# Optimization experiments

Hardware: AMD Instinct MI355X
Metric: run time of the kernel (lower is better)

The kernel has to match this reference:

```python
import jax, jax.numpy as jnp
import numpy as np

N_HEADS = 16
N_KV_HEADS = 4
HEAD_DIM = 128


def apply_rotary_emb(x, cos, sin):
    # x: [B, S, H, D]; cos/sin: [S, D//2]
    xr = x[..., 0::2]
    xi = x[..., 1::2]
    c = cos[None, :, None, :]
    s = sin[None, :, None, :]
    out_r = xr * c - xi * s
    out_i = xr * s + xi * c
    # interleave back: [..., D//2, 2] -> [..., D]
    return jnp.stack([out_r, out_i], axis=-1).reshape(x.shape)


def setup_inputs() -> dict:
    key = jax.random.key(0)
    ks = jax.random.split(key, 7)
    B, S, D = 4, 2048, 2048
    x = jax.random.normal(ks[0], (B, S, D), dtype=jnp.float32)
    # realistic rotary tables
    inv_freq = 1.0 / (10000.0 ** (jnp.arange(0, HEAD_DIM, 2, dtype=jnp.float32) / HEAD_DIM))
    t = jnp.arange(S, dtype=jnp.float32)
    freqs = jnp.outer(t, inv_freq)  # [S, D/2]
    freqs_cos = jnp.cos(freqs)
    freqs_sin = jnp.sin(freqs)
    sc = 0.02
    wq = jax.random.normal(ks[1], (D, N_HEADS * HEAD_DIM), dtype=jnp.float32) * sc
    wk = jax.random.normal(ks[2], (D, N_KV_HEADS * HEAD_DIM), dtype=jnp.float32) * sc
    wv = jax.random.normal(ks[3], (D, N_KV_HEADS * HEAD_DIM), dtype=jnp.float32) * sc
    wo = jax.random.normal(ks[4], (N_HEADS * HEAD_DIM, D), dtype=jnp.float32) * sc
    return {"x": x, "freqs_cos": freqs_cos, "freqs_sin": freqs_sin,
            "wq": wq, "wk": wk, "wv": wv, "wo": wo}


def reference(x, freqs_cos, freqs_sin, wq, wk, wv, wo):
    B, S, D = x.shape
    n_rep = N_HEADS // N_KV_HEADS
    xq = (x @ wq).reshape(B, S, N_HEADS, HEAD_DIM)
    xk = (x @ wk).reshape(B, S, N_KV_HEADS, HEAD_DIM)
    xv = (x @ wv).reshape(B, S, N_KV_HEADS, HEAD_DIM)
    xq = apply_rotary_emb(xq, freqs_cos, freqs_sin)
    xk = apply_rotary_emb(xk, freqs_cos, freqs_sin)
    # repeat_kv (GQA): [B,S,Hkv,D] -> [B,S,Hkv*n_rep,D]
    xk = jnp.repeat(xk, n_rep, axis=2)
    xv = jnp.repeat(xv, n_rep, axis=2)
    # [B,H,S,D]
    q = xq.transpose(0, 2, 1, 3)
    k = xk.transpose(0, 2, 1, 3)
    v = xv.transpose(0, 2, 1, 3)
    scores = jnp.einsum('bhqd,bhkd->bhqk', q, k) / jnp.sqrt(jnp.float32(HEAD_DIM))
    causal = jnp.triu(jnp.ones((S, S), dtype=bool), k=1)
    scores = jnp.where(causal[None, None], -jnp.inf, scores)
    probs = jax.nn.softmax(scores, axis=-1)
    out = jnp.einsum('bhqk,bhkd->bhqd', probs, v)
    out = out.transpose(0, 2, 1, 3).reshape(B, S, N_HEADS * HEAD_DIM)
    return out @ wo
```

## Files before the change

kernel.cpp:

```cpp
#include <hip/hip_runtime.h>
#include <stdint.h>
#include <stddef.h>

#define B_ 4
#define S_ 2048
#define D_ 2048
#define NH 16
#define NKV 4
#define HD 128
#define QKV_N 3072
#define ROWS (B_*S_)

typedef unsigned short u16;
typedef __attribute__((ext_vector_type(8))) unsigned short u16x8;
typedef __attribute__((ext_vector_type(8))) __bf16 bf16x8;
typedef __attribute__((ext_vector_type(4))) float f32x4;

__device__ __forceinline__ u16 f2bf(float f) {
  unsigned u = __builtin_bit_cast(unsigned, f);
  return (u16)((u + 0x7fffu + ((u >> 16) & 1u)) >> 16);
}
__device__ __forceinline__ float bf2f(u16 h) {
  return __builtin_bit_cast(float, (unsigned)h << 16);
}
__device__ __forceinline__ f32x4 mfma16(u16x8 a, u16x8 b, f32x4 c) {
  return __builtin_amdgcn_mfma_f32_16x16x32_bf16(
      __builtin_bit_cast(bf16x8, a), __builtin_bit_cast(bf16x8, b), c, 0, 0, 0);
}
__device__ __forceinline__ void gld16(const void* g, void* l) {
  __builtin_amdgcn_global_load_lds(
      (const __attribute__((address_space(1))) void*)g,
      (__attribute__((address_space(3))) void*)l, 16, 0, 0);
}

__global__ __launch_bounds__(256) void k_cast_x(const float* __restrict__ x, u16* __restrict__ xb) {
  int i = blockIdx.x * 256 + threadIdx.x;
  float4 v = ((const float4*)x)[i];
  union { u16 u[4]; uint2 p; } o;
  o.u[0] = f2bf(v.x); o.u[1] = f2bf(v.y); o.u[2] = f2bf(v.z); o.u[3] = f2bf(v.w);
  ((uint2*)xb)[i] = o.p;
}

__global__ __launch_bounds__(256) void k_wt(const float* __restrict__ w, u16* __restrict__ wt, int K, int N) {
  __shared__ float tile[32][33];
  int kb = blockIdx.y * 32, nb = blockIdx.x * 32;
  int tx = threadIdx.x, ty = threadIdx.y;
#pragma unroll
  for (int j = 0; j < 32; j += 8)
    tile[ty + j][tx] = w[(size_t)(kb + ty + j) * N + nb + tx];
  __syncthreads();
#pragma unroll
  for (int j = 0; j < 32; j += 8)
    wt[(size_t)(nb + ty + j) * K + kb + tx] = f2bf(tile[tx][ty + j]);
}

template<int NT, bool F32OUT>
__global__ __launch_bounds__(256) void k_gemm(const u16* __restrict__ A, const u16* __restrict__ Bt,
                                              void* __restrict__ C) {
  const int K = 2048;
  __shared__ u16 As[128 * 32];
  __shared__ u16 Bs[128 * 32];
  int mb = blockIdx.y * 128, nb = blockIdx.x * 128;
  int t = threadIdx.x;
  int l = t & 63, lane16 = l & 15, quad = l >> 4;
  int w = t >> 6;
  int wm = (w >> 1) * 64, wn = (w & 1) * 64;
  f32x4 acc[4][4] = {};
  for (int k0 = 0; k0 < K; k0 += 32) {
#pragma unroll
    for (int p = 0; p < 2; ++p) {
      int lin = p * 256 + t;
      int row = lin >> 2, ch = lin & 3;
      gld16(A  + (size_t)(mb + row) * K + k0 + ch * 8, As + (p * 256 + (t & 192)) * 8);
      gld16(Bt + (size_t)(nb + row) * K + k0 + ch * 8, Bs + (p * 256 + (t & 192)) * 8);
    }
    __syncthreads();
    u16x8 af[4], bf[4];
#pragma unroll
    for (int mt = 0; mt < 4; ++mt)
      af[mt] = *(const u16x8*)(As + (wm + mt * 16 + lane16) * 32 + quad * 8);
#pragma unroll
    for (int nt = 0; nt < 4; ++nt)
      bf[nt] = *(const u16x8*)(Bs + (wn + nt * 16 + lane16) * 32 + quad * 8);
#pragma unroll
    for (int mt = 0; mt < 4; ++mt)
#pragma unroll
      for (int nt = 0; nt < 4; ++nt)
        acc[mt][nt] = mfma16(af[mt], bf[nt], acc[mt][nt]);
    __syncthreads();
  }
#pragma unroll
  for (int mt = 0; mt < 4; ++mt)
#pragma unroll
    for (int nt = 0; nt < 4; ++nt)
#pragma unroll
      for (int r = 0; r < 4; ++r) {
        int row = mb + wm + mt * 16 + quad * 4 + r;
        int col = nb + wn + nt * 16 + lane16;
        if constexpr (F32OUT)
          ((float*)C)[(size_t)row * NT + col] = acc[mt][nt][r];
        else
          ((u16*)C)[(size_t)row * NT + col] = f2bf(acc[mt][nt][r]);
      }
}

__global__ __launch_bounds__(256) void k_rope(const u16* __restrict__ qkv, const float* __restrict__ fc,
                                              const float* __restrict__ fs, u16* __restrict__ Q,
                                              u16* __restrict__ Kk) {
  const float SC = 0.1275174214f;
  int row = blockIdx.x;
  int b = row >> 11, s = row & 2047;
  int t = threadIdx.x;
#pragma unroll
  for (int j = 0; j < 5; ++j) {
    int p = t + j * 256;
    int i = p & 63;
    float c = fc[s * 64 + i], sn = fs[s * 64 + i];
    if (p < 1024) {
      int h = p >> 6;
      unsigned pr = *(const unsigned*)(qkv + (size_t)row * QKV_N + h * 128 + 2 * i);
      float xr = bf2f((u16)(pr & 0xffff)), xi = bf2f((u16)(pr >> 16));
      size_t o = (((size_t)(b * NH + h) * S_) + s) * HD + 2 * i;
      unsigned out = (unsigned)f2bf((xr * c - xi * sn) * SC) |
                     ((unsigned)f2bf((xr * sn + xi * c) * SC) << 16);
      *(unsigned*)(Q + o) = out;
    } else {
      int kh = (p - 1024) >> 6;
      unsigned pr = *(const unsigned*)(qkv + (size_t)row * QKV_N + 2048 + kh * 128 + 2 * i);
      float xr = bf2f((u16)(pr & 0xffff)), xi = bf2f((u16)(pr >> 16));
      size_t o = (((size_t)(b * NKV + kh) * S_) + s) * HD + 2 * i;
      unsigned out = (unsigned)f2bf(xr * c - xi * sn) | ((unsigned)f2bf(xr * sn + xi * c) << 16);
      *(unsigned*)(Kk + o) = out;
    }
  }
}

__global__ __launch_bounds__(256) void k_vt(const u16* __restrict__ qkv, u16* __restrict__ Vt) {
  __shared__ u16 tile[64 * 128];
  int blk = blockIdx.x;
  int sb = blk & 31, kh = (blk >> 5) & 3, b = blk >> 7;
  int t = threadIdx.x;
  int s0 = sb * 64;
#pragma unroll
  for (int i = 0; i < 4; ++i) {
    int lin = i * 256 + t;
    int row = lin >> 4, c = lin & 15;
    u16x8 v = *(const u16x8*)(qkv + (size_t)(b * S_ + s0 + row) * QKV_N + 2560 + kh * HD + c * 8);
    *(u16x8*)(tile + row * 128 + ((c ^ (row & 15)) * 8)) = v;
  }
  __syncthreads();
#pragma unroll
  for (int i = 0; i < 2; ++i) {
    int u = i * 256 + t;
    int p = u >> 3, o = u & 7;
    u16 lo[8], hi[8];
#pragma unroll
    for (int j = 0; j < 8; ++j) {
      int s = o * 8 + j;
      int cs = (p >> 2) ^ (s & 15);
      unsigned v = *(const unsigned*)(tile + s * 128 + cs * 8 + (p & 3) * 2);
      lo[j] = (u16)(v & 0xffff); hi[j] = (u16)(v >> 16);
    }
    size_t ob = ((size_t)(b * NKV + kh) * HD + 2 * p) * S_ + s0 + o * 8;
    *(u16x8*)(Vt + ob)      = *(u16x8*)lo;
    *(u16x8*)(Vt + ob + S_) = *(u16x8*)hi;
  }
}

__global__ __launch_bounds__(256) void k_attn(const u16* __restrict__ Q, const u16* __restrict__ Kg,
                                              const u16* __restrict__ Vt, u16* __restrict__ O) {
  int bx = blockIdx.x;
  int bh = bx >> 3, pr = bx & 7;
  int b = bh >> 4, h = bh & 15, kh = h >> 2;
  int t = threadIdx.x;
  int w = t >> 6, l = t & 63, L = l & 15, quad = l >> 4;

  __shared__ u16 Ks[64 * 128];
  __shared__ u16 Vs[128 * 64];
  __shared__ u16 Ps[4][32 * 72];
  u16* Pw = &Ps[w][0];

  const u16* Qh = Q  + ((size_t)(b * NH  + h ) * S_) * HD;
  const u16* Kh = Kg + ((size_t)(b * NKV + kh) * S_) * HD;
  const u16* Vh = Vt + ((size_t)(b * NKV + kh) * HD) * S_;

  u16x8 ones;
#pragma unroll
  for (int i = 0; i < 8; ++i) ones[i] = 0x3F80;

  int koff[4], voff[2];
#pragma unroll
  for (int kk = 0; kk < 4; ++kk) koff[kk] = 128 * L + 8 * ((4 * kk + quad) ^ (L & 7));
#pragma unroll
  for (int kc = 0; kc < 2; ++kc) voff[kc] = 64 * L + 8 * ((4 * kc + quad) ^ (L & 7));
  const int pread  = 72 * L + 8 * quad;
  const int pwrite = 72 * L + 4 * quad;

  int kgo[4], vgo[4], klo[4], vlo[4];
#pragma unroll
  for (int i = 0; i < 4; ++i) {
    int lin = i * 256 + t;
    int row = lin >> 4, c = lin & 15;
    kgo[i] = row * HD + ((c ^ (row & 7)) * 8);
    int d = lin >> 3, c2 = lin & 7;
    vgo[i] = d * S_ + ((c2 ^ (d & 7)) * 8);
    klo[i] = (i * 256 + (t & 192)) * 8;
    vlo[i] = (i * 256 + (t & 192)) * 8;
  }

#pragma unroll 1
  for (int half = 0; half < 2; ++half) {
    int qb = half ? (15 - pr) : pr;
    int q0 = qb * 128 + w * 32;

    u16x8 qf[2][4];
#pragma unroll
    for (int m = 0; m < 2; ++m)
#pragma unroll
      for (int kk = 0; kk < 4; ++kk)
        qf[m][kk] = *(const u16x8*)(Qh + (size_t)(q0 + m * 16 + L) * HD + kk * 32 + quad * 8);

    f32x4 acc[2][9] = {};
    int ktiles = 2 * qb + 2;
#pragma unroll 1
    for (int kt = 0; kt < ktiles; ++kt) {
      int kbase = kt * 64;
      __syncthreads();
      const u16* Kt = Kh + (size_t)kbase * HD;
      const u16* Vg = Vh + kbase;
#pragma unroll
      for (int i = 0; i < 4; ++i) gld16(Kt + kgo[i], Ks + klo[i]);
#pragma unroll
      for (int i = 0; i < 4; ++i) gld16(Vg + vgo[i], Vs + vlo[i]);
      __syncthreads();
      if (kbase > q0 + 31) continue;

      bool needMask = (kbase + 63 > q0);
#pragma unroll
      for (int n = 0; n < 4; ++n) {
        f32x4 s0v = {}, s1v = {};
#pragma unroll
        for (int kk = 0; kk < 4; ++kk) {
          u16x8 kf = *(const u16x8*)(Ks + koff[kk] + 2048 * n);
          s0v = mfma16(kf, qf[0][kk], s0v);
          s1v = mfma16(kf, qf[1][kk], s1v);
        }
#pragma unroll
        for (int m = 0; m < 2; ++m) {
          f32x4 sv = m ? s1v : s0v;
          int qrow = q0 + m * 16 + L;
          unsigned eu[4];
#pragma unroll
          for (int r = 0; r < 4; ++r) {
            float e = exp2f(sv[r]);
            if (needMask) {
              int key = kbase + n * 16 + quad * 4 + r;
              e = (key <= qrow) ? e : 0.0f;
            }
            eu[r] = __builtin_bit_cast(unsigned, e);
          }
          uint2 pk;
          pk.x = __builtin_amdgcn_perm(eu[1], eu[0], 0x07060302u);
          pk.y = __builtin_amdgcn_perm(eu[3], eu[2], 0x07060302u);
          *(uint2*)(Pw + pwrite + 1152 * m + 16 * n) = pk;
        }
      }
#pragma unroll
      for (int kc = 0; kc < 2; ++kc) {
        u16x8 pf0 = *(const u16x8*)(Pw + pread + 32 * kc);
        u16x8 pf1 = *(const u16x8*)(Pw + pread + 1152 + 32 * kc);
#pragma unroll
        for (int nt = 0; nt < 8; ++nt) {
          u16x8 vf = *(const u16x8*)(Vs + voff[kc] + 1024 * nt);
          acc[0][nt] = mfma16(pf0, vf, acc[0][nt]);
          acc[1][nt] = mfma16(pf1, vf, acc[1][nt]);
        }
        acc[0][8] = mfma16(pf0, ones, acc[0][8]);
        acc[1][8] = mfma16(pf1, ones, acc[1][8]);
      }
    }
#pragma unroll
    for (int m = 0; m < 2; ++m)
#pragma unroll
      for (int r = 0; r < 4; ++r) {
        float inv = 1.0f / acc[m][8][r];
        int qrow = q0 + m * 16 + quad * 4 + r;
#pragma unroll
        for (int nt = 0; nt < 8; ++nt) {
          int col = h * HD + nt * 16 + L;
          O[(size_t)(b * S_ + qrow) * D_ + col] = f2bf(acc[m][nt][r] * inv);
        }
      }
  }
}

extern "C" void kernel_launch(void* const* d_in, const int* in_sizes, int n_in,
                              void* d_out, int out_size, void* d_ws, size_t ws_size,
                              hipStream_t stream) {
  const float* x  = (const float*)d_in[0];
  const float* fc = (const float*)d_in[1];
  const float* fs = (const float*)d_in[2];
  const float* wq = (const float*)d_in[3];
  const float* wk = (const float*)d_in[4];
  const float* wv = (const float*)d_in[5];
  const float* wo = (const float*)d_in[6];
  float* out = (float*)d_out;

  u16* p = (u16*)d_ws;
  u16* xb    = p; p += (size_t)ROWS * D_;
  u16* wqkvT = p; p += (size_t)QKV_N * D_;
  u16* woT   = p; p += (size_t)D_ * D_;
  u16* qkv   = p; p += (size_t)ROWS * QKV_N;
  u16* Qr    = p; p += (size_t)ROWS * (NH * HD);
  u16* Kr    = p; p += (size_t)ROWS * (NKV * HD);
  u16* Vtr   = p; p += (size_t)ROWS * (NKV * HD);
  u16* AO    = p; p += (size_t)ROWS * D_;

  k_cast_x<<<dim3(ROWS * D_ / 1024), dim3(256), 0, stream>>>(x, xb);
  k_wt<<<dim3(64, 64), dim3(32, 8), 0, stream>>>(wq, wqkvT, 2048, 2048);
  k_wt<<<dim3(16, 64), dim3(32, 8), 0, stream>>>(wk, wqkvT + (size_t)2048 * 2048, 2048, 512);
  k_wt<<<dim3(16, 64), dim3(32, 8), 0, stream>>>(wv, wqkvT + (size_t)2560 * 2048, 2048, 512);
  k_wt<<<dim3(64, 64), dim3(32, 8), 0, stream>>>(wo, woT, 2048, 2048);
  k_gemm<QKV_N, false><<<dim3(QKV_N / 128, ROWS / 128), dim3(256), 0, stream>>>(xb, wqkvT, qkv);
  k_rope<<<dim3(ROWS), dim3(256), 0, stream>>>(qkv, fc, fs, Qr, Kr);
  k_vt<<<dim3(B_ * NKV * (S_ / 64)), dim3(256), 0, stream>>>(qkv, Vtr);
  k_attn<<<dim3(64 * 8), dim3(256), 0, stream>>>(Qr, Kr, Vtr, AO);
  k_gemm<D_, true><<<dim3(D_ / 128, ROWS / 128), dim3(256), 0, stream>>>(AO, woT, out);
}
```

Measured before the change: 500.4 us.

## Rewrite bf16 GEMM with 256x256 tiles, multi-stage LDS pipeline, swizzle and XCD remap

Replaces the simple single-buffer 128x128 GEMM with a 512-thread, 256x256-tile kernel. It keeps a 4-stage global-to-LDS pipeline with explicit vmcnt waits and barriers, and XOR-swizzles LDS chunks to avoid bank conflicts. It also raises MFMA priority via s_setprio and remaps block IDs across XCDs for L2 locality. This is meant to hide load latency and raise MFMA utilisation for the QKV and output projections. In exchange it uses much more LDS and registers, and it relies on hand-counted waitcnts being correct.

Measured after the change: 466.2 us. 6.8% less time.

```diff
diff --git a/kernel.cpp b/kernel.cpp
--- a/kernel.cpp
+++ b/kernel.cpp
@@ -54,53 +54,99 @@
     wt[(size_t)(nb + ty + j) * K + kb + tx] = f2bf(tile[tx][ty + j]);
 }
 
+
+#define STG_A(KK, SS) do {                                                   \
+    gld16(Ag + (size_t)r0 * 2048 + (KK) + coff, As + (SS) * 8192 + stl0);    \
+    gld16(Ag + (size_t)(r0 + 128) * 2048 + (KK) + coff,                      \
+          As + (SS) * 8192 + stl1);                                          \
+  } while (0)
+#define STG_B(KK, SS) do {                                                   \
+    gld16(Bg + (size_t)r0 * 2048 + (KK) + coff, Bs + (SS) * 8192 + stl0);    \
+    gld16(Bg + (size_t)(r0 + 128) * 2048 + (KK) + coff,                      \
+          Bs + (SS) * 8192 + stl1);                                          \
+  } while (0)
+
+#define PHASE(RS, MB, RB, SS, SK, SA, VM) do {                               \
+    if (SA) STG_A(SK, SS); else STG_B(SK, SS);                               \
+    const u16* Ap_ = As + (RS) * 8192;                                       \
+    _Pragma("unroll") for (int i_ = 0; i_ < 4; ++i_)                         \
+      af[i_] = *(const u16x8*)(Ap_ + arow0 + ((MB) + i_) * 512);             \
+    if (RB) {                                                                \
+      const u16* Bp_ = Bs + (RS) * 8192;                                     \
+      _Pragma("unroll") for (int i_ = 0; i_ < 4; ++i_)                       \
+        bf[i_] = *(const u16x8*)(Bp_ + brow0 + i_ * 512);                    \
+    }                                                                        \
+    __builtin_amdgcn_s_setprio(1);                                           \
+    _Pragma("unroll") for (int i_ = 0; i_ < 4; ++i_)                         \
+      _Pragma("unroll") for (int n_ = 0; n_ < 4; ++n_)                       \
+        acc[(MB) + i_][n_] = mfma16(af[i_], bf[n_], acc[(MB) + i_][n_]);     \
+    __builtin_amdgcn_s_setprio(0);                                           \
+    if (VM) asm volatile("s_waitcnt vmcnt(8)" ::: "memory");                 \
+    asm volatile("s_barrier" ::: "memory");                                  \
+  } while (0)
+
 template<int NT, bool F32OUT>
-__global__ __launch_bounds__(256) void k_gemm(const u16* __restrict__ A, const u16* __restrict__ Bt,
-                                              void* __restrict__ C) {
-  const int K = 2048;
-  __shared__ u16 As[128 * 32];
-  __shared__ u16 Bs[128 * 32];
-  int mb = blockIdx.y * 128, nb = blockIdx.x * 128;
+__global__ __launch_bounds__(512, 2) void k_gemm(const u16* __restrict__ A, const u16* __restrict__ Bt,
+                                                 void* __restrict__ C) {
+  __shared__ u16 As[4 * 8192];
+  __shared__ u16 Bs[4 * 8192];
+  int id = blockIdx.x;
+  int nwg = gridDim.x;
+  id = (id & 7) * (nwg >> 3) + (id >> 3);
+  const int gx = NT / 256;
+  int mb = (id / gx) * 256, nb = (id % gx) * 256;
+
   int t = threadIdx.x;
-  int l = t & 63, lane16 = l & 15, quad = l >> 4;
-  int w = t >> 6;
-  int wm = (w >> 1) * 64, wn = (w & 1) * 64;
-  f32x4 acc[4][4] = {};
-  for (int k0 = 0; k0 < K; k0 += 32) {
-#pragma unroll
-    for (int p = 0; p < 2; ++p) {
-      int lin = p * 256 + t;
-      int row = lin >> 2, ch = lin & 3;
-      gld16(A  + (size_t)(mb + row) * K + k0 + ch * 8, As + (p * 256 + (t & 192)) * 8);
-      gld16(Bt + (size_t)(nb + row) * K + k0 + ch * 8, Bs + (p * 256 + (t & 192)) * 8);
-    }
-    __syncthreads();
-    u16x8 af[4], bf[4];
-#pragma unroll
-    for (int mt = 0; mt < 4; ++mt)
-      af[mt] = *(const u16x8*)(As + (wm + mt * 16 + lane16) * 32 + quad * 8);
-#pragma unroll
-    for (int nt = 0; nt < 4; ++nt)
-      bf[nt] = *(const u16x8*)(Bs + (wn + nt * 16 + lane16) * 32 + quad * 8);
-#pragma unroll
-    for (int mt = 0; mt < 4; ++mt)
-#pragma unroll
-      for (int nt = 0; nt < 4; ++nt)
-        acc[mt][nt] = mfma16(af[mt], bf[nt], acc[mt][nt]);
-    __syncthreads();
-  }
-#pragma unroll
-  for (int mt = 0; mt < 4; ++mt)
-#pragma unroll
-    for (int nt = 0; nt < 4; ++nt)
+  int l = t & 63, L16 = l & 15, quad = l >> 4;
+  int w = t >> 6, wm = w >> 2, wn = w & 3;
+  const int schunk = 8 * (quad ^ (L16 & 3));
+  const int arow0 = (wm * 128 + L16) * 32 + schunk;
+  const int brow0 = (wn * 64 + L16) * 32 + schunk;
+  const int r0 = t >> 2;
+  const int coff = 8 * ((t & 3) ^ (r0 & 3));
+  const int stl0 = (t & 448) * 8, stl1 = stl0 + 4096;
+
+  const u16* Ag = A + (size_t)mb * 2048;
+  const u16* Bg = Bt + (size_t)nb * 2048;
+  u16x8 af[4], bf[4];
+  f32x4 acc[8][4] = {};
+
+  STG_A(0, 0);  STG_B(0, 0);
+  STG_A(32, 1); STG_B(32, 1);
+  STG_A(64, 2); STG_B(64, 2);
+  asm volatile("s_waitcnt vmcnt(8)" ::: "memory");
+  asm volatile("s_barrier" ::: "memory");
+
+#pragma unroll 1
+  for (int tp = 0; tp < 16; ++tp) {
+    int t0 = tp * 2;
+    int ka1 = ((t0 + 1) & 31) * 64 + 32;
+    int ka2 = ((t0 + 2) & 31) * 64;
+    int kb1 = ((t0 + 2) & 31) * 64 + 32;
+    int kb2 = ((t0 + 3) & 31) * 64;
+    PHASE(0, 0, true,  3, ka1, true,  false);
+    PHASE(0, 4, false, 3, ka1, false, true);
+    PHASE(1, 0, true,  0, ka2, true,  false);
+    PHASE(1, 4, false, 0, ka2, false, true);
+    PHASE(2, 0, true,  1, kb1, true,  false);
+    PHASE(2, 4, false, 1, kb1, false, true);
+    PHASE(3, 0, true,  2, kb2, true,  false);
+    PHASE(3, 4, false, 2, kb2, false, true);
+  }
+  asm volatile("s_waitcnt vmcnt(0)" ::: "memory");
+
+#pragma unroll
+  for (int m = 0; m < 8; ++m)
+#pragma unroll
+    for (int n = 0; n < 4; ++n)
 #pragma unroll
       for (int r = 0; r < 4; ++r) {
-        int row = mb + wm + mt * 16 + quad * 4 + r;
-        int col = nb + wn + nt * 16 + lane16;
+        int row = mb + wm * 128 + m * 16 + quad * 4 + r;
+        int col = nb + wn * 64 + n * 16 + L16;
         if constexpr (F32OUT)
-          ((float*)C)[(size_t)row * NT + col] = acc[mt][nt][r];
+          ((float*)C)[(size_t)row * NT + col] = acc[m][n][r];
         else
-          ((u16*)C)[(size_t)row * NT + col] = f2bf(acc[mt][nt][r]);
+          ((u16*)C)[(size_t)row * NT + col] = f2bf(acc[m][n][r]);
       }
 }
 
@@ -321,9 +367,9 @@
   k_wt<<<dim3(16, 64), dim3(32, 8), 0, stream>>>(wk, wqkvT + (size_t)2048 * 2048, 2048, 512);
   k_wt<<<dim3(16, 64), dim3(32, 8), 0, stream>>>(wv, wqkvT + (size_t)2560 * 2048, 2048, 512);
   k_wt<<<dim3(64, 64), dim3(32, 8), 0, stream>>>(wo, woT, 2048, 2048);
-  k_gemm<QKV_N, false><<<dim3(QKV_N / 128, ROWS / 128), dim3(256), 0, stream>>>(xb, wqkvT, qkv);
+  k_gemm<QKV_N, false><<<dim3((QKV_N / 256) * (ROWS / 256)), dim3(512), 0, stream>>>(xb, wqkvT, qkv);
   k_rope<<<dim3(ROWS), dim3(256), 0, stream>>>(qkv, fc, fs, Qr, Kr);
   k_vt<<<dim3(B_ * NKV * (S_ / 64)), dim3(256), 0, stream>>>(qkv, Vtr);
   k_attn<<<dim3(64 * 8), dim3(256), 0, stream>>>(Qr, Kr, Vtr, AO);
-  k_gemm<D_, true><<<dim3(D_ / 128, ROWS / 128), dim3(256), 0, stream>>>(AO, woT, out);
-}
+  k_gemm<D_, true><<<dim3((D_ / 256) * (ROWS / 256)), dim3(512), 0, stream>>>(AO, woT, out);
+}
```
